# Performance work log

Measured on AMD Instinct MI355X. Metric: run time of the kernel, lower is better.

Reference implementation:

```python
import jax, jax.numpy as jnp
import numpy as np

T, B, H = 2048, 64, 256   # time, batch, hidden/input/memory size
A = 256                   # attention_size
IN = H + H                # cell input size = input_size + memory_size = 512
NEG = -1e12


def setup_inputs() -> dict:
    key = jax.random.key(0)
    ks = jax.random.split(key, 12)
    s = lambda k, shape, fan: jax.random.normal(k, shape, jnp.float32) / np.sqrt(fan)
    inp = {
        "input": jax.random.normal(ks[0], (B, H), jnp.float32),
        "memory": jax.random.normal(ks[1], (T, B, H), jnp.float32),
        "memory_mask": jax.random.bernoulli(ks[2], 0.9, (T, B)),
        "state": jax.random.normal(ks[3], (B, H), jnp.float32),
        # attention MLP: Linear(input+state+memory -> A, no bias), Tanh, Linear(A -> 1, no bias)
        "W_a1": s(ks[4], (H + H + H, A), H * 3),
        "w_a2": s(ks[5], (A,), A),
        # gate: Linear(IN -> IN, no bias) + sigmoid
        "W_gate": s(ks[6], (IN, IN), IN),
        # GRUCell params (torch layout: [3H, in], gates order r,z,n)
        "W_ih": s(ks[7], (3 * H, IN), IN),
        "W_hh": s(ks[8], (3 * H, H), H),
        "b_ih": jnp.zeros((3 * H,), jnp.float32),
        "b_hh": jnp.zeros((3 * H,), jnp.float32),
    }
    return inp


def reference(input, memory, memory_mask, state, W_a1, w_a2, W_gate, W_ih, W_hh, b_ih, b_hh):
    # --- additive attention: tanh(W1 @ [input, state, memory]) @ w2 ---
    # split W_a1 by the concat layout [input | state | memory]
    qs = jnp.concatenate([input, state], axis=-1) @ W_a1[: 2 * H]      # [B, A]
    mp = jnp.einsum("tbh,ha->tba", memory, W_a1[2 * H :])               # [T, B, A]
    logits = jnp.tanh(qs[None] + mp) @ w_a2                              # [T, B]
    logits = jnp.where(memory_mask, logits, NEG)
    scores = jax.nn.softmax(logits, axis=0)                              # [T, B]
    attn_vec = jnp.einsum("tb,tbh->bh", scores, memory)                  # [B, H]

    # --- gate ---
    new_input = jnp.concatenate([input, attn_vec], axis=-1)              # [B, 2H]
    gated = new_input * jax.nn.sigmoid(new_input @ W_gate)

    # --- GRU cell (torch semantics, gates r, z, n) ---
    gi = gated @ W_ih.T + b_ih                                           # [B, 3H]
    gh = state @ W_hh.T + b_hh                                           # [B, 3H]
    i_r, i_z, i_n = jnp.split(gi, 3, axis=-1)
    h_r, h_z, h_n = jnp.split(gh, 3, axis=-1)
    r = jax.nn.sigmoid(i_r + h_r)
    z = jax.nn.sigmoid(i_z + h_z)
    n = jnp.tanh(i_n + r * h_n)
    return (1.0 - z) * n + z * state                                     # [B, H]
```

## Files before the change

### kernel.cpp

```cpp
#include <hip/hip_runtime.h>
#include <hip/hip_bf16.h>

#define B_DIM 64
#define H_DIM 256
#define NCHG 4
#define CHUNKS 8
#define TCH 64

typedef __attribute__((ext_vector_type(8))) short short8;
typedef __attribute__((ext_vector_type(4))) float f32x4;

__device__ __forceinline__ unsigned short bfbits(float f) {
    __hip_bfloat16 h = __float2bfloat16(f);
    unsigned short u;
    __builtin_memcpy(&u, &h, 2);
    return u;
}
__device__ __forceinline__ float fexp(float x) {
    float r;
    asm("v_exp_f32 %0, %1" : "=v"(r) : "v"(x * 1.4426950408889634f));
    return r;
}
__device__ __forceinline__ float ftanh(float x) {
    float e, r;
    asm("v_exp_f32 %0, %1" : "=v"(e) : "v"(x * 2.8853900817779268f));
    asm("v_rcp_f32 %0, %1" : "=v"(r) : "v"(e + 1.0f));
    return 1.0f - 2.0f * r;
}
__device__ __forceinline__ float fast_sigmoid(float x) {
    return 1.0f / (1.0f + __expf(-x));
}
__device__ __forceinline__ void lds_barrier() {
    asm volatile("s_waitcnt lgkmcnt(0)" ::: "memory");
    __builtin_amdgcn_s_barrier();
    __builtin_amdgcn_sched_barrier(0);
}

__global__ void prep_qs_kernel(const float* __restrict__ W_a1,
                               const float* __restrict__ input,
                               const float* __restrict__ state,
                               unsigned short* __restrict__ WmT,
                               float* __restrict__ qs) {
    __shared__ float cat[512];
    int bid = blockIdx.x, tid = threadIdx.x;
    if (bid < 256) {
        WmT[tid * 256 + bid] = bfbits(W_a1[(512 + bid) * 256 + tid]);
    } else {
        int b = bid - 256;
        cat[tid] = input[b * 256 + tid];
        cat[256 + tid] = state[b * 256 + tid];
        __syncthreads();
        int a = tid;
        float s0 = 0.f, s1 = 0.f, s2 = 0.f, s3 = 0.f;
        #pragma unroll 4
        for (int k = 0; k < 512; k += 4) {
            s0 += cat[k]     * W_a1[(k)     * 256 + a];
            s1 += cat[k + 1] * W_a1[(k + 1) * 256 + a];
            s2 += cat[k + 2] * W_a1[(k + 2) * 256 + a];
            s3 += cat[k + 3] * W_a1[(k + 3) * 256 + a];
        }
        qs[b * 256 + a] = (s0 + s1) + (s2 + s3);
    }
}

__global__ __launch_bounds__(512, 1) void attn_kernel(
    const float* __restrict__ memory, const int* __restrict__ mask,
    const unsigned short* __restrict__ WmT,
    const float* __restrict__ qs, const float* __restrict__ w_a2,
    float* __restrict__ part_l, float* __restrict__ part_acc)
{
    extern __shared__ char smem[];
    unsigned short* slab0 = (unsigned short*)smem;
    unsigned short* slab1 = (unsigned short*)(smem + 32768);
    float* lpart = (float*)(smem + 65536);
    int*   maskL = (int*)(smem + 65536 + 2048);

    int b = blockIdx.x, g = blockIdx.y;
    int tid = threadIdx.x;
    int lane = tid & 63, w = tid >> 6;
    int lr = lane & 15, lh = lane >> 4;
    int tbase = g * (CHUNKS * TCH);
    const float* mbase = memory + (size_t)tbase * (B_DIM * H_DIM) + b * H_DIM;

    int wa0 = w * 32;
    short8 areg[8][2];
    #pragma unroll
    for (int kk = 0; kk < 8; ++kk)
        #pragma unroll
        for (int mf = 0; mf < 2; ++mf)
            areg[kk][mf] = *(const short8*)(WmT + (wa0 + mf * 16 + lr) * 256 + kk * 32 + lh * 8);

    float qv[2][4], wv[2][4];
    #pragma unroll
    for (int mf = 0; mf < 2; ++mf)
        #pragma unroll
        for (int r = 0; r < 4; ++r) {
            int a = wa0 + mf * 16 + lh * 4 + r;
            qv[mf][r] = qs[b * 256 + a];
            wv[mf][r] = w_a2[a];
        }

    maskL[tid] = mask[(tbase + tid) * B_DIM + b];

    int wby = (lane * 8) ^ (w << 4);

    float4 ldA[8], ldB[8];
#define ISSUE(dst, q)                                                          \
    _Pragma("unroll") for (int i = 0; i < 8; ++i)                              \
        dst[i] = *((const float4*)(mbase + (size_t)((q) * TCH + i * 8 + w) *   \
                                   (B_DIM * H_DIM)) + lane);
#define WRITE(src, sl)                                                         \
    _Pragma("unroll") for (int i = 0; i < 8; ++i) {                            \
        ushort4 o;                                                             \
        o.x = bfbits(src[i].x); o.y = bfbits(src[i].y);                        \
        o.z = bfbits(src[i].z); o.w = bfbits(src[i].w);                        \
        *(ushort4*)((char*)(sl) + (i * 8 + w) * 512 + wby) = o;                \
    }

    ISSUE(ldA, 0)
    WRITE(ldA, slab0)
    ISSUE(ldB, 1)
    lds_barrier();

    float a8[8] = {0.f, 0.f, 0.f, 0.f, 0.f, 0.f, 0.f, 0.f};
    float l_acc = 0.f;
    int slice4 = ((lane >> 5) + 2 * w) * 4;
    int hpvb = (lane & 31) * 16;

    #pragma unroll
    for (int s = 0; s < CHUNKS; ++s) {
        char* curp = (char*)((s & 1) ? slab1 : slab0);
        char* nxtp = (char*)((s & 1) ? slab0 : slab1);
        const char* cur = curp;

        if (s + 2 < CHUNKS) {
            if ((s & 1) == 0) { ISSUE(ldA, s + 2) }
            else              { ISSUE(ldB, s + 2) }
        }

        f32x4 acc[2][4];
        #pragma unroll
        for (int mf = 0; mf < 2; ++mf)
            #pragma unroll
            for (int nf = 0; nf < 4; ++nf)
                acc[mf][nf] = (f32x4){0.f, 0.f, 0.f, 0.f};
        #pragma unroll
        for (int kk = 0; kk < 8; ++kk) {
            int kbyte = kk * 64 + lh * 16;
            #pragma unroll
            for (int nf = 0; nf < 4; ++nf) {
                int t = nf * 16 + lr;
                int sw = kbyte ^ ((t & 7) << 4);
                short8 bfr = *(const short8*)(cur + t * 512 + sw);
                acc[0][nf] = __builtin_amdgcn_mfma_f32_16x16x32_bf16(areg[kk][0], bfr, acc[0][nf], 0, 0, 0);
                acc[1][nf] = __builtin_amdgcn_mfma_f32_16x16x32_bf16(areg[kk][1], bfr, acc[1][nf], 0, 0, 0);
            }
        }

        if (s + 1 < CHUNKS) {
            if ((s & 1) == 0) { WRITE(ldB, nxtp) }
            else              { WRITE(ldA, nxtp) }
        }

        #pragma unroll
        for (int nf = 0; nf < 4; ++nf) {
            float sv = 0.f;
            #pragma unroll
            for (int mf = 0; mf < 2; ++mf)
                #pragma unroll
                for (int r = 0; r < 4; ++r)
                    sv += wv[mf][r] * ftanh(qv[mf][r] + acc[mf][nf][r]);
            sv += __shfl_xor(sv, 16);
            sv += __shfl_xor(sv, 32);
            if (lh == 0) lpart[w * 64 + nf * 16 + lr] = sv;
        }
        lds_barrier();

        float lg = 0.f;
        #pragma unroll
        for (int ww = 0; ww < 8; ++ww) lg += lpart[ww * 64 + lane];
        float pself = maskL[s * 64 + lane] ? fexp(lg) : 0.f;
        if (w == 0) l_acc += pself;

        #pragma unroll
        for (int tt = 0; tt < 4; ++tt) {
            int tl = slice4 + tt;
            float pt = __shfl(pself, tl);
            int swb = hpvb ^ ((tl & 7) << 4);
            uint4 u = *(const uint4*)(cur + tl * 512 + swb);
            a8[0] += pt * __uint_as_float(u.x << 16);
            a8[1] += pt * __uint_as_float(u.x & 0xFFFF0000u);
            a8[2] += pt * __uint_as_float(u.y << 16);
            a8[3] += pt * __uint_as_float(u.y & 0xFFFF0000u);
            a8[4] += pt * __uint_as_float(u.z << 16);
            a8[5] += pt * __uint_as_float(u.z & 0xFFFF0000u);
            a8[6] += pt * __uint_as_float(u.w << 16);
            a8[7] += pt * __uint_as_float(u.w & 0xFFFF0000u);
        }
        lds_barrier();
    }
#undef ISSUE
#undef WRITE

    __syncthreads();
    float* acc2 = (float*)smem;
    int oct = lane & 31, slice = 2 * w + (lane >> 5), h0 = oct * 8;
    *(float4*)(&acc2[slice * 256 + h0])     = (float4){a8[0], a8[1], a8[2], a8[3]};
    *(float4*)(&acc2[slice * 256 + h0 + 4]) = (float4){a8[4], a8[5], a8[6], a8[7]};
    __syncthreads();
    int pidx = g * B_DIM + b;
    if (tid < 256) {
        float ssum = 0.f;
        #pragma unroll
        for (int sl = 0; sl < 16; ++sl) ssum += acc2[sl * 256 + tid];
        part_acc[(size_t)pidx * 256 + tid] = ssum;
    }
    if (w == 0) {
        #pragma unroll
        for (int d = 1; d < 64; d <<= 1) l_acc += __shfl_xor(l_acc, d);
        if (lane == 0) part_l[pidx] = l_acc;
    }
}

__global__ void mergegate_kernel(const float* __restrict__ part_l,
                                 const float* __restrict__ part_acc,
                                 const float* __restrict__ input,
                                 const float* __restrict__ W_gate,
                                 float* __restrict__ gated) {
    __shared__ float ni[512];
    int b = blockIdx.x, tid = threadIdx.x;
    if (tid >= 256) {
        int k = tid - 256;
        ni[k] = input[b * 256 + k];
    } else {
        int h = tid;
        float L = 0.f, s = 0.f;
        #pragma unroll
        for (int c = 0; c < NCHG; ++c) {
            L += part_l[c * 64 + b];
            s += part_acc[(size_t)(c * 64 + b) * 256 + h];
        }
        ni[256 + h] = s / L;
    }
    __syncthreads();
    int j = tid;
    float s0 = 0.f, s1 = 0.f, s2 = 0.f, s3 = 0.f;
    #pragma unroll 4
    for (int k = 0; k < 512; k += 4) {
        s0 += ni[k]     * W_gate[(k)     * 512 + j];
        s1 += ni[k + 1] * W_gate[(k + 1) * 512 + j];
        s2 += ni[k + 2] * W_gate[(k + 2) * 512 + j];
        s3 += ni[k + 3] * W_gate[(k + 3) * 512 + j];
    }
    float s = (s0 + s1) + (s2 + s3);
    gated[b * 512 + j] = ni[j] * fast_sigmoid(s);
}

__global__ __launch_bounds__(768) void gru_kernel(
    const float* __restrict__ gated, const float* __restrict__ state,
    const float* __restrict__ W_ih, const float* __restrict__ W_hh,
    const float* __restrict__ b_ih, const float* __restrict__ b_hh,
    float* __restrict__ out) {
    __shared__ float ld_g[4][512];
    __shared__ float ld_s[4][256];
    __shared__ float xi[3][16][4];
    __shared__ float xh[3][16][4];
    int ht = blockIdx.x & 15, bt = blockIdx.x >> 4;
    int tid = threadIdx.x;
    #pragma unroll
    for (int i = 0; i < 3; ++i) {
        int idx = i * 768 + tid;
        if (idx < 2048) ld_g[idx >> 9][idx & 511] = gated[(bt * 4 + (idx >> 9)) * 512 + (idx & 511)];
    }
    #pragma unroll
    for (int i = 0; i < 2; ++i) {
        int idx = i * 768 + tid;
        if (idx < 1024) ld_s[idx >> 8][idx & 255] = state[(bt * 4 + (idx >> 8)) * 256 + (idx & 255)];
    }

    int gid = tid >> 4, lk = tid & 15;
    int gate = gid >> 4, hl = gid & 15;
    int j = gate * 256 + ht * 16 + hl;

    float4 wi[8], wh[4];
    #pragma unroll
    for (int it = 0; it < 8; ++it)
        wi[it] = *(const float4*)(W_ih + (size_t)j * 512 + it * 64 + lk * 4);
    #pragma unroll
    for (int it = 0; it < 4; ++it)
        wh[it] = *(const float4*)(W_hh + (size_t)j * 256 + it * 64 + lk * 4);
    float bi = b_ih[j], bh = b_hh[j];
    __syncthreads();

    #pragma unroll
    for (int bb = 0; bb < 4; ++bb) {
        float g0 = 0.f, g1 = 0.f;
        #pragma unroll
        for (int it = 0; it < 8; ++it) {
            float4 gv = *(const float4*)(&ld_g[bb][it * 64 + lk * 4]);
            g0 += wi[it].x * gv.x + wi[it].z * gv.z;
            g1 += wi[it].y * gv.y + wi[it].w * gv.w;
        }
        float h0 = 0.f, h1 = 0.f;
        #pragma unroll
        for (int it = 0; it < 4; ++it) {
            float4 sv = *(const float4*)(&ld_s[bb][it * 64 + lk * 4]);
            h0 += wh[it].x * sv.x + wh[it].z * sv.z;
            h1 += wh[it].y * sv.y + wh[it].w * sv.w;
        }
        float gi_ = g0 + g1, gh_ = h0 + h1;
        #pragma unroll
        for (int m = 1; m < 16; m <<= 1) {
            gi_ += __shfl_xor(gi_, m);
            gh_ += __shfl_xor(gh_, m);
        }
        if (lk == 0) { xi[gate][hl][bb] = gi_ + bi; xh[gate][hl][bb] = gh_ + bh; }
    }
    __syncthreads();
    if (tid < 64) {
        int bb = tid >> 4, hl2 = tid & 15;
        float ir = xi[0][hl2][bb], hr = xh[0][hl2][bb];
        float iz = xi[1][hl2][bb], hz = xh[1][hl2][bb];
        float in_ = xi[2][hl2][bb], hn = xh[2][hl2][bb];
        float r = fast_sigmoid(ir + hr);
        float z = fast_sigmoid(iz + hz);
        float n = 1.0f - 2.0f / (__expf(2.0f * (in_ + r * hn)) + 1.0f);
        out[(bt * 4 + bb) * 256 + ht * 16 + hl2] =
            (1.f - z) * n + z * ld_s[bb][ht * 16 + hl2];
    }
}

extern "C" void kernel_launch(void* const* d_in, const int* in_sizes, int n_in,
                              void* d_out, int out_size, void* d_ws, size_t ws_size,
                              hipStream_t stream) {
    const float* input  = (const float*)d_in[0];
    const float* memory = (const float*)d_in[1];
    const int*   mask   = (const int*)d_in[2];
    const float* state  = (const float*)d_in[3];
    const float* W_a1   = (const float*)d_in[4];
    const float* w_a2   = (const float*)d_in[5];
    const float* W_gate = (const float*)d_in[6];
    const float* W_ih   = (const float*)d_in[7];
    const float* W_hh   = (const float*)d_in[8];
    const float* b_ih   = (const float*)d_in[9];
    const float* b_hh   = (const float*)d_in[10];
    float* out = (float*)d_out;

    char* ws = (char*)d_ws;
    unsigned short* WmT = (unsigned short*)(ws + 0);
    float* qs       = (float*)(ws + 131072);
    float* gated    = (float*)(ws + 196608);
    float* part_l   = (float*)(ws + 327680);
    float* part_acc = (float*)(ws + 335872);

    prep_qs_kernel<<<320, 256, 0, stream>>>(W_a1, input, state, WmT, qs);

    (void)hipFuncSetAttribute((const void*)attn_kernel,
                              hipFuncAttributeMaxDynamicSharedMemorySize, 69632);
    attn_kernel<<<dim3(B_DIM, NCHG), 512, 69632, stream>>>(
        memory, mask, WmT, qs, w_a2, part_l, part_acc);

    mergegate_kernel<<<64, 512, 0, stream>>>(part_l, part_acc, input, W_gate, gated);
    gru_kernel<<<256, 768, 0, stream>>>(gated, state, W_ih, W_hh, b_ih, b_hh, out);
}
```

Measured before the change: 94.22 us.

## Double grid time-splits, single register buffer, allow two blocks per CU

Splits the time axis across eight chunk groups instead of four, giving 512 attention blocks in place of 256. The register double buffer of memory loads becomes a single buffer and the loop is no longer fully unrolled. Launch bounds now allow two blocks per CU, and the LDS allocation shrinks so two blocks can fit. Sigmoid and tanh in the gate and GRU kernels switch to raw exp and rcp instructions. The aim is better occupancy and latency hiding on the memory-bound attention pass. In exchange, prefetch distance drops to one chunk, and the merge step has more partial results to combine.

```diff
diff --git a/kernel.cpp b/kernel.cpp
--- a/kernel.cpp
+++ b/kernel.cpp
@@ -3,8 +3,8 @@
 
 #define B_DIM 64
 #define H_DIM 256
-#define NCHG 4
-#define CHUNKS 8
+#define NCHG 8
+#define CHUNKS 4
 #define TCH 64
 
 typedef __attribute__((ext_vector_type(8))) short short8;
@@ -27,8 +27,11 @@
     asm("v_rcp_f32 %0, %1" : "=v"(r) : "v"(e + 1.0f));
     return 1.0f - 2.0f * r;
 }
-__device__ __forceinline__ float fast_sigmoid(float x) {
-    return 1.0f / (1.0f + __expf(-x));
+__device__ __forceinline__ float fsigmoid(float x) {
+    float e, r;
+    asm("v_exp_f32 %0, %1" : "=v"(e) : "v"(x * -1.4426950408889634f));
+    asm("v_rcp_f32 %0, %1" : "=v"(r) : "v"(e + 1.0f));
+    return r;
 }
 __device__ __forceinline__ void lds_barrier() {
     asm volatile("s_waitcnt lgkmcnt(0)" ::: "memory");
@@ -63,7 +66,7 @@
     }
 }
 
-__global__ __launch_bounds__(512, 1) void attn_kernel(
+__global__ __launch_bounds__(512, 2) void attn_kernel(
     const float* __restrict__ memory, const int* __restrict__ mask,
     const unsigned short* __restrict__ WmT,
     const float* __restrict__ qs, const float* __restrict__ w_a2,
@@ -100,43 +103,38 @@
             wv[mf][r] = w_a2[a];
         }
 
-    maskL[tid] = mask[(tbase + tid) * B_DIM + b];
+    if (tid < CHUNKS * TCH) maskL[tid] = mask[(tbase + tid) * B_DIM + b];
 
     int wby = (lane * 8) ^ (w << 4);
 
-    float4 ldA[8], ldB[8];
-#define ISSUE(dst, q)                                                          \
+    float4 ld[8];
+#define ISSUE(q)                                                               \
     _Pragma("unroll") for (int i = 0; i < 8; ++i)                              \
-        dst[i] = *((const float4*)(mbase + (size_t)((q) * TCH + i * 8 + w) *   \
-                                   (B_DIM * H_DIM)) + lane);
-#define WRITE(src, sl)                                                         \
+        ld[i] = *((const float4*)(mbase + (size_t)((q) * TCH + i * 8 + w) *    \
+                                  (B_DIM * H_DIM)) + lane);
+#define WRITE(sl)                                                              \
     _Pragma("unroll") for (int i = 0; i < 8; ++i) {                            \
         ushort4 o;                                                             \
-        o.x = bfbits(src[i].x); o.y = bfbits(src[i].y);                        \
-        o.z = bfbits(src[i].z); o.w = bfbits(src[i].w);                        \
+        o.x = bfbits(ld[i].x); o.y = bfbits(ld[i].y);                          \
+        o.z = bfbits(ld[i].z); o.w = bfbits(ld[i].w);                          \
         *(ushort4*)((char*)(sl) + (i * 8 + w) * 512 + wby) = o;                \
     }
 
-    ISSUE(ldA, 0)
-    WRITE(ldA, slab0)
-    ISSUE(ldB, 1)
-    lds_barrier();
+    ISSUE(0)
+    WRITE(slab0)
 
     float a8[8] = {0.f, 0.f, 0.f, 0.f, 0.f, 0.f, 0.f, 0.f};
     float l_acc = 0.f;
     int slice4 = ((lane >> 5) + 2 * w) * 4;
     int hpvb = (lane & 31) * 16;
 
-    #pragma unroll
     for (int s = 0; s < CHUNKS; ++s) {
-        char* curp = (char*)((s & 1) ? slab1 : slab0);
-        char* nxtp = (char*)((s & 1) ? slab0 : slab1);
-        const char* cur = curp;
-
-        if (s + 2 < CHUNKS) {
-            if ((s & 1) == 0) { ISSUE(ldA, s + 2) }
-            else              { ISSUE(ldB, s + 2) }
-        }
+        const char* cur = (const char*)((s & 1) ? slab1 : slab0);
+        char* nxt = (char*)((s & 1) ? slab0 : slab1);
+
+        lds_barrier();
+
+        if (s + 1 < CHUNKS) { ISSUE(s + 1) }
 
         f32x4 acc[2][4];
         #pragma unroll
@@ -155,11 +153,6 @@
                 acc[0][nf] = __builtin_amdgcn_mfma_f32_16x16x32_bf16(areg[kk][0], bfr, acc[0][nf], 0, 0, 0);
                 acc[1][nf] = __builtin_amdgcn_mfma_f32_16x16x32_bf16(areg[kk][1], bfr, acc[1][nf], 0, 0, 0);
             }
-        }
-
-        if (s + 1 < CHUNKS) {
-            if ((s & 1) == 0) { WRITE(ldB, nxtp) }
-            else              { WRITE(ldA, nxtp) }
         }
 
         #pragma unroll
@@ -197,7 +190,8 @@
             a8[6] += pt * __uint_as_float(u.w << 16);
             a8[7] += pt * __uint_as_float(u.w & 0xFFFF0000u);
         }
-        lds_barrier();
+
+        if (s + 1 < CHUNKS) { WRITE(nxt) }
     }
 #undef ISSUE
 #undef WRITE
@@ -253,7 +247,7 @@
         s3 += ni[k + 3] * W_gate[(k + 3) * 512 + j];
     }
     float s = (s0 + s1) + (s2 + s3);
-    gated[b * 512 + j] = ni[j] * fast_sigmoid(s);
+    gated[b * 512 + j] = ni[j] * fsigmoid(s);
 }
 
 __global__ __launch_bounds__(768) void gru_kernel(
@@ -322,9 +316,9 @@
         float ir = xi[0][hl2][bb], hr = xh[0][hl2][bb];
         float iz = xi[1][hl2][bb], hz = xh[1][hl2][bb];
         float in_ = xi[2][hl2][bb], hn = xh[2][hl2][bb];
-        float r = fast_sigmoid(ir + hr);
-        float z = fast_sigmoid(iz + hz);
-        float n = 1.0f - 2.0f / (__expf(2.0f * (in_ + r * hn)) + 1.0f);
+        float r = fsigmoid(ir + hr);
+        float z = fsigmoid(iz + hz);
+        float n = ftanh(in_ + r * hn);
         out[(bt * 4 + bb) * 256 + ht * 16 + hl2] =
             (1.f - z) * n + z * ld_s[bb][ht * 16 + hl2];
     }
@@ -356,8 +350,8 @@
     prep_qs_kernel<<<320, 256, 0, stream>>>(W_a1, input, state, WmT, qs);
 
     (void)hipFuncSetAttribute((const void*)attn_kernel,
-                              hipFuncAttributeMaxDynamicSharedMemorySize, 69632);
-    attn_kernel<<<dim3(B_DIM, NCHG), 512, 69632, stream>>>(
+                              hipFuncAttributeMaxDynamicSharedMemorySize, 68608);
+    attn_kernel<<<dim3(B_DIM, NCHG), 512, 68608, stream>>>(
         memory, mask, WmT, qs, w_a2, part_l, part_acc);
 
     mergegate_kernel<<<64, 512, 0, stream>>>(part_l, part_acc, input, W_gate, gated);
```

Result: faster. 78.60 us (-16.6%).
